# Optimization experiments

Measured on AMD Instinct MI355X. Metric: run time of the kernel, lower is better.

Reference implementation:

```python
import jax, jax.numpy as jnp
import numpy as np

HEAD_SIZE = 128  # matches init head_size; original scales by global head_size**-0.5


def setup_inputs() -> dict:
    key = jax.random.key(0)
    k1, k2, k3, k4 = jax.random.split(key, 4)
    B, T, C, D = 16, 2048, 1024, HEAD_SIZE
    x = jax.random.normal(k1, (B, T, C), dtype=jnp.float32)
    # torch Linear weight is [out,in]; store transposed so forward is x @ W
    Wq = jax.random.normal(k2, (C, D), dtype=jnp.float32) * (C ** -0.5)
    Wk = jax.random.normal(k3, (C, D), dtype=jnp.float32) * (C ** -0.5)
    Wv = jax.random.normal(k4, (C, D), dtype=jnp.float32) * (C ** -0.5)
    return {"x": x, "Wq": Wq, "Wk": Wk, "Wv": Wv}


def reference(x, Wq, Wk, Wv):
    # x: [B,T,C]; projections -> [B,T,D]
    q = x @ Wq
    k = x @ Wk
    v = x @ Wv
    T = x.shape[1]
    scale = HEAD_SIZE ** -0.5
    # scores: [B,T,T]
    wei = jnp.einsum("btd,bsd->bts", q, k) * scale
    causal = jnp.tril(jnp.ones((T, T), dtype=bool))  # tril buffer
    wei = jnp.where(causal, wei, -jnp.inf)
    wei = jax.nn.softmax(wei, axis=-1)
    # dropout is identity in eval mode (deterministic reference)
    return wei @ v  # [B,T,D]
```

## Files before the change

### kernel.cpp

```cpp
#include <hip/hip_runtime.h>
#include <hip/hip_bf16.h>

typedef short bf16x8 __attribute__((ext_vector_type(8)));
typedef float f32x4 __attribute__((ext_vector_type(4)));
typedef unsigned short u16x4 __attribute__((ext_vector_type(4)));

#define B_ 16
#define T_ 2048
#define C_ 1024
#define D_ 128
#define M_ (B_ * T_)

static __device__ __forceinline__ unsigned short f2bf(float f) {
    unsigned int u = __builtin_bit_cast(unsigned int, f);
    unsigned int r = (u + 0x7fffu + ((u >> 16) & 1u)) >> 16;
    return (unsigned short)r;
}

static __device__ __forceinline__ void gll16(const unsigned short* g, unsigned short* l) {
    __builtin_amdgcn_global_load_lds(
        (const __attribute__((address_space(1))) void*)g,
        (__attribute__((address_space(3))) void*)l, 16, 0, 0);
}

#define TPAD 133

__global__ void wt_kernel(const float* __restrict__ Wq, const float* __restrict__ Wk,
                          const float* __restrict__ Wv, unsigned short* __restrict__ Wt) {
    __shared__ float Tl[64 * TPAD];
    const int o  = blockIdx.x >> 4;
    const int k0 = (blockIdx.x & 15) * 64;
    const float* W = (o == 0) ? Wq : (o == 1) ? Wk : Wv;
    const int tid = threadIdx.x;

    const int kr = tid >> 5;
    const int n4 = (tid & 31) * 4;
#pragma unroll
    for (int j = 0; j < 8; ++j) {
        float4 v = *(const float4*)(W + (size_t)(k0 + kr + j * 8) * 128 + n4);
        *(float4*)&Tl[(kr + j * 8) * TPAD + n4] = v;
    }
    __syncthreads();

    const int nb = tid >> 3;
    const int kg = (tid & 7) * 8;
#pragma unroll
    for (int j = 0; j < 4; ++j) {
        const int nn = nb + j * 32;
        const int kk = kg ^ ((nn & 7) * 8);
        bf16x8 v;
#pragma unroll
        for (int e = 0; e < 8; ++e)
            v[e] = (short)f2bf(Tl[(kk + e) * TPAD + nn]);
        *(bf16x8*)&Wt[((size_t)o * 128 + nn) * 1024 + k0 + kg] = v;
    }
}

#define ASTR 68

__launch_bounds__(512, 2)
__global__ void qkv_kernel(const float* __restrict__ x, const unsigned short* __restrict__ Wt,
                           unsigned short* __restrict__ Q, unsigned short* __restrict__ K,
                           unsigned short* __restrict__ Vt) {
    __shared__ unsigned short Alds[2][128 * ASTR];
    __shared__ unsigned short Blds[2][384 * 64];

    const int tid  = threadIdx.x;
    const int lane = tid & 63;
    const int w    = tid >> 6;
    const int wr   = w >> 2;
    const int wc   = w & 3;
    const int lr   = lane & 15;
    const int lk   = lane >> 4;
    const int m0   = blockIdx.x * 128;

    const int axr = tid >> 4;
    const int axc = (tid & 15) * 4;

    float4 ar[4];
    auto loadA = [&](int k0) {
#pragma unroll
        for (int j = 0; j < 4; ++j)
            ar[j] = *(const float4*)(x + (size_t)(m0 + axr + j * 32) * C_ + k0 + axc);
    };
    auto writeA = [&](int buf) {
#pragma unroll
        for (int j = 0; j < 4; ++j) {
            u16x4 v;
            v[0] = f2bf(ar[j].x); v[1] = f2bf(ar[j].y);
            v[2] = f2bf(ar[j].z); v[3] = f2bf(ar[j].w);
            *(u16x4*)&Alds[buf][(axr + j * 32) * ASTR + axc] = v;
        }
    };

    auto stageB = [&](int k0, int buf) {
#pragma unroll
        for (int c = 0; c < 6; ++c) {
            const int chunk = w * 6 + c;
            const unsigned short* g = Wt + (size_t)(chunk * 8 + (lane >> 3)) * 1024
                                         + k0 + (lane & 7) * 8;
            gll16(g, &Blds[buf][chunk * 512]);
        }
    };

    f32x4 acc[4][6] = {};

    auto compute = [&](int buf) {
#pragma unroll
        for (int kk = 0; kk < 2; ++kk) {
            bf16x8 a[4], b[6];
#pragma unroll
            for (int rb = 0; rb < 4; ++rb)
                a[rb] = *(bf16x8*)&Alds[buf][(wr * 64 + rb * 16 + lr) * ASTR + kk * 32 + lk * 8];
#pragma unroll
            for (int nb = 0; nb < 6; ++nb) {
                const int ng = wc * 96 + nb * 16 + lr;
                b[nb] = *(bf16x8*)&Blds[buf][ng * 64 + ((kk * 32 + lk * 8) ^ ((ng & 7) * 8))];
            }
#pragma unroll
            for (int rb = 0; rb < 4; ++rb)
#pragma unroll
                for (int nb = 0; nb < 6; ++nb)
                    acc[rb][nb] = __builtin_amdgcn_mfma_f32_16x16x32_bf16(a[rb], b[nb], acc[rb][nb], 0, 0, 0);
        }
    };

    stageB(0, 0);
    loadA(0);
    writeA(0);

    for (int t = 0; t < 16; ++t) {
        __syncthreads();
        const int cur = t & 1;
        if (t < 15) {
            stageB((t + 1) * 64, cur ^ 1);
            loadA((t + 1) * 64);
        }
        compute(cur);
        if (t < 15) writeA(cur ^ 1);
    }

    const float qscale = 0.08838834764831845f;
    const int b  = m0 / T_;
    const int t0 = m0 % T_;
#pragma unroll
    for (int rb = 0; rb < 4; ++rb) {
#pragma unroll
        for (int nb = 0; nb < 6; ++nb) {
            const int row0 = wr * 64 + rb * 16 + lk * 4;
            const int col  = wc * 96 + nb * 16 + lr;
            const int o    = col >> 7;
            const int d    = col & 127;
            f32x4 a = acc[rb][nb];
            if (o == 0) {
#pragma unroll
                for (int r = 0; r < 4; ++r)
                    Q[(size_t)(m0 + row0 + r) * D_ + d] = f2bf(a[r] * qscale);
            } else if (o == 1) {
#pragma unroll
                for (int r = 0; r < 4; ++r)
                    K[(size_t)(m0 + row0 + r) * D_ + d] = f2bf(a[r]);
            } else {
                u16x4 pv;
#pragma unroll
                for (int r = 0; r < 4; ++r) pv[r] = f2bf(a[r]);
                *(u16x4*)&Vt[((size_t)b * D_ + d) * T_ + t0 + row0] = pv;
            }
        }
    }
}

#define KSTR 132
#define VSTR 68
#define PSTR 68

__launch_bounds__(256, 2)
__global__ void attn_kernel(const unsigned short* __restrict__ Q, const unsigned short* __restrict__ K,
                            const unsigned short* __restrict__ Vt, float* __restrict__ out) {
    __shared__ unsigned short Klds[2][64 * KSTR];
    __shared__ unsigned short Vlds[2][128 * VSTR];
    __shared__ unsigned short Plds[4][16 * PSTR];

    const int tid  = threadIdx.x;
    const int lane = tid & 63;
    const int w    = tid >> 6;
    const int lr   = lane & 15;
    const int lk   = lane >> 4;

    int bid = blockIdx.x;
    int batch, qt;
    if (bid < 256) { batch = bid >> 4; qt = bid & 15; }
    else           { bid -= 256; batch = bid >> 4; qt = 31 - (bid & 15); }

    const unsigned short* Qb = Q  + (size_t)batch * T_ * D_;
    const unsigned short* Kb = K  + (size_t)batch * T_ * D_;
    const unsigned short* Vb = Vt + (size_t)batch * D_ * T_;
    float* outb = out + (size_t)batch * T_ * D_;

    const int kxr = tid >> 4;
    const int kxc = (tid & 15) * 8;
    const int vxr = tid >> 3;
    const int vxc = (tid & 7) * 8;

    bf16x8 kr[4], vr[4];
    auto kv_load = [&](int kvt) {
        const int kv0 = kvt * 64;
#pragma unroll
        for (int j = 0; j < 4; ++j)
            kr[j] = *(const bf16x8*)(Kb + (size_t)(kv0 + kxr + j * 16) * D_ + kxc);
#pragma unroll
        for (int j = 0; j < 4; ++j)
            vr[j] = *(const bf16x8*)(Vb + (size_t)(vxr + j * 32) * T_ + kv0 + vxc);
    };
    auto kv_write = [&](int buf) {
#pragma unroll
        for (int j = 0; j < 4; ++j)
            *(bf16x8*)&Klds[buf][(kxr + j * 16) * KSTR + kxc] = kr[j];
#pragma unroll
        for (int j = 0; j < 4; ++j)
            *(bf16x8*)&Vlds[buf][(vxr + j * 32) * VSTR + vxc] = vr[j];
    };

    const int qw = qt * 64 + w * 16;

    bf16x8 qf[4];
#pragma unroll
    for (int c = 0; c < 4; ++c)
        qf[c] = *(const bf16x8*)(Qb + (size_t)(qw + lr) * D_ + lk * 8 + c * 32);

    f32x4 o_acc[8] = {};
    float mrun[4] = {-1e30f, -1e30f, -1e30f, -1e30f};
    float lrun[4] = {0.f, 0.f, 0.f, 0.f};

    kv_load(0);
    kv_write(0);

    for (int kvt = 0; kvt <= qt; ++kvt) {
        const int cur = kvt & 1;
        __syncthreads();
        if (kvt < qt) kv_load(kvt + 1);

        f32x4 s[4];
#pragma unroll
        for (int nb = 0; nb < 4; ++nb) {
            f32x4 a = {};
#pragma unroll
            for (int c = 0; c < 4; ++c) {
                bf16x8 kf = *(bf16x8*)&Klds[cur][(nb * 16 + lr) * KSTR + lk * 8 + c * 32];
                a = __builtin_amdgcn_mfma_f32_16x16x32_bf16(qf[c], kf, a, 0, 0, 0);
            }
            s[nb] = a;
        }

        if (kvt == qt) {
#pragma unroll
            for (int nb = 0; nb < 4; ++nb)
#pragma unroll
                for (int r = 0; r < 4; ++r) {
                    int qg = qw + lk * 4 + r;
                    int kg = kvt * 64 + nb * 16 + lr;
                    if (kg > qg) s[nb][r] = -1e30f;
                }
        }

        float scale_[4];
#pragma unroll
        for (int r = 0; r < 4; ++r) {
            float mx = fmaxf(fmaxf(s[0][r], s[1][r]), fmaxf(s[2][r], s[3][r]));
            mx = fmaxf(mx, __shfl_xor(mx, 1));
            mx = fmaxf(mx, __shfl_xor(mx, 2));
            mx = fmaxf(mx, __shfl_xor(mx, 4));
            mx = fmaxf(mx, __shfl_xor(mx, 8));
            float mnew = fmaxf(mrun[r], mx);
            scale_[r]  = __expf(mrun[r] - mnew);
            mrun[r]    = mnew;
            lrun[r]   *= scale_[r];
        }
#pragma unroll
        for (int db = 0; db < 8; ++db)
#pragma unroll
            for (int r = 0; r < 4; ++r) o_acc[db][r] *= scale_[r];

#pragma unroll
        for (int nb = 0; nb < 4; ++nb)
#pragma unroll
            for (int r = 0; r < 4; ++r) {
                float p = __expf(s[nb][r] - mrun[r]);
                lrun[r] += p;
                Plds[w][(lk * 4 + r) * PSTR + nb * 16 + lr] = f2bf(p);
            }
        asm volatile("s_waitcnt lgkmcnt(0)" ::: "memory");
        __builtin_amdgcn_sched_barrier(0);

        bf16x8 pa[2];
#pragma unroll
        for (int c = 0; c < 2; ++c)
            pa[c] = *(bf16x8*)&Plds[w][lr * PSTR + lk * 8 + c * 32];
#pragma unroll
        for (int db = 0; db < 8; ++db) {
            f32x4 oo = o_acc[db];
#pragma unroll
            for (int c = 0; c < 2; ++c) {
                bf16x8 vf = *(bf16x8*)&Vlds[cur][(db * 16 + lr) * VSTR + lk * 8 + c * 32];
                oo = __builtin_amdgcn_mfma_f32_16x16x32_bf16(pa[c], vf, oo, 0, 0, 0);
            }
            o_acc[db] = oo;
        }

        if (kvt < qt) kv_write(cur ^ 1);
    }

#pragma unroll
    for (int r = 0; r < 4; ++r) {
        float sgm = lrun[r];
        sgm += __shfl_xor(sgm, 1);
        sgm += __shfl_xor(sgm, 2);
        sgm += __shfl_xor(sgm, 4);
        sgm += __shfl_xor(sgm, 8);
        lrun[r] = 1.0f / sgm;
    }
#pragma unroll
    for (int db = 0; db < 8; ++db)
#pragma unroll
        for (int r = 0; r < 4; ++r)
            outb[(size_t)(qw + lk * 4 + r) * D_ + db * 16 + lr] = o_acc[db][r] * lrun[r];
}

extern "C" void kernel_launch(void* const* d_in, const int* in_sizes, int n_in,
                              void* d_out, int out_size, void* d_ws, size_t ws_size,
                              hipStream_t stream) {
    const float* x  = (const float*)d_in[0];
    const float* Wq = (const float*)d_in[1];
    const float* Wk = (const float*)d_in[2];
    const float* Wv = (const float*)d_in[3];

    unsigned short* Wt  = (unsigned short*)d_ws;
    unsigned short* Qw  = (unsigned short*)((char*)d_ws + (1 << 20));
    unsigned short* Kw  = Qw + (size_t)M_ * D_;
    unsigned short* Vtw = Kw + (size_t)M_ * D_;

    hipLaunchKernelGGL(wt_kernel, dim3(48), dim3(256), 0, stream, Wq, Wk, Wv, Wt);
    hipLaunchKernelGGL(qkv_kernel, dim3(256), dim3(512), 0, stream, x, Wt, Qw, Kw, Vtw);
    hipLaunchKernelGGL(attn_kernel, dim3(512), dim3(256), 0, stream, Qw, Kw, Vtw, (float*)d_out);
}
```

Measured before the change: 105.8 us.

## Restructure QKV projection: full-K x tile in LDS, weights pre-tiled for direct MFMA loads

The weight-prep kernel now writes the bf16 weights in a fragment-tiled layout so each lane can load its MFMA B operand straight from global memory (L2-resident) without staging in LDS. The QKV kernel now loads a 64-row slab of x over the full K dimension, converts it to bf16 in LDS once, and runs the whole K loop with no double buffering or per-step barriers. The grid doubles to 512 blocks of 64 rows, and each wave computes 48 output columns. This removes the per-iteration sync and staging overhead. In exchange it uses about 131KB of LDS per block (one block per CU), does not overlap the x load with compute, and makes every block re-read all weights from cache.

```diff
diff --git a/kernel.cpp b/kernel.cpp
--- a/kernel.cpp
+++ b/kernel.cpp
@@ -17,16 +17,10 @@
     return (unsigned short)r;
 }
 
-static __device__ __forceinline__ void gll16(const unsigned short* g, unsigned short* l) {
-    __builtin_amdgcn_global_load_lds(
-        (const __attribute__((address_space(1))) void*)g,
-        (__attribute__((address_space(3))) void*)l, 16, 0, 0);
-}
-
 #define TPAD 133
 
 __global__ void wt_kernel(const float* __restrict__ Wq, const float* __restrict__ Wk,
-                          const float* __restrict__ Wv, unsigned short* __restrict__ Wt) {
+                          const float* __restrict__ Wv, unsigned short* __restrict__ Wt2) {
     __shared__ float Tl[64 * TPAD];
     const int o  = blockIdx.x >> 4;
     const int k0 = (blockIdx.x & 15) * 64;
@@ -42,102 +36,62 @@
     }
     __syncthreads();
 
-    const int nb = tid >> 3;
-    const int kg = (tid & 7) * 8;
+    const int n    = tid & 127;
+    const int half = tid >> 7;
 #pragma unroll
     for (int j = 0; j < 4; ++j) {
-        const int nn = nb + j * 32;
-        const int kk = kg ^ ((nn & 7) * 8);
+        const int kg = half * 4 + j;
         bf16x8 v;
 #pragma unroll
         for (int e = 0; e < 8; ++e)
-            v[e] = (short)f2bf(Tl[(kk + e) * TPAD + nn]);
-        *(bf16x8*)&Wt[((size_t)o * 128 + nn) * 1024 + k0 + kg] = v;
-    }
-}
-
-#define ASTR 68
-
-__launch_bounds__(512, 2)
-__global__ void qkv_kernel(const float* __restrict__ x, const unsigned short* __restrict__ Wt,
+            v[e] = (short)f2bf(Tl[(kg * 8 + e) * TPAD + n]);
+        const int nblk = o * 8 + (n >> 4);
+        const int kblk = (k0 >> 3) + kg;
+        *(bf16x8*)&Wt2[((size_t)nblk * 128 + kblk) * 128 + (n & 15) * 8] = v;
+    }
+}
+
+#define XSTR 1026
+
+__launch_bounds__(512, 1)
+__global__ void qkv_kernel(const float* __restrict__ x, const unsigned short* __restrict__ Wt2,
                            unsigned short* __restrict__ Q, unsigned short* __restrict__ K,
                            unsigned short* __restrict__ Vt) {
-    __shared__ unsigned short Alds[2][128 * ASTR];
-    __shared__ unsigned short Blds[2][384 * 64];
+    __shared__ unsigned short X[64 * XSTR];
 
     const int tid  = threadIdx.x;
     const int lane = tid & 63;
     const int w    = tid >> 6;
-    const int wr   = w >> 2;
-    const int wc   = w & 3;
     const int lr   = lane & 15;
     const int lk   = lane >> 4;
-    const int m0   = blockIdx.x * 128;
-
-    const int axr = tid >> 4;
-    const int axc = (tid & 15) * 4;
-
-    float4 ar[4];
-    auto loadA = [&](int k0) {
-#pragma unroll
-        for (int j = 0; j < 4; ++j)
-            ar[j] = *(const float4*)(x + (size_t)(m0 + axr + j * 32) * C_ + k0 + axc);
-    };
-    auto writeA = [&](int buf) {
-#pragma unroll
-        for (int j = 0; j < 4; ++j) {
-            u16x4 v;
-            v[0] = f2bf(ar[j].x); v[1] = f2bf(ar[j].y);
-            v[2] = f2bf(ar[j].z); v[3] = f2bf(ar[j].w);
-            *(u16x4*)&Alds[buf][(axr + j * 32) * ASTR + axc] = v;
-        }
-    };
-
-    auto stageB = [&](int k0, int buf) {
-#pragma unroll
-        for (int c = 0; c < 6; ++c) {
-            const int chunk = w * 6 + c;
-            const unsigned short* g = Wt + (size_t)(chunk * 8 + (lane >> 3)) * 1024
-                                         + k0 + (lane & 7) * 8;
-            gll16(g, &Blds[buf][chunk * 512]);
-        }
-    };
-
-    f32x4 acc[4][6] = {};
-
-    auto compute = [&](int buf) {
-#pragma unroll
-        for (int kk = 0; kk < 2; ++kk) {
-            bf16x8 a[4], b[6];
-#pragma unroll
-            for (int rb = 0; rb < 4; ++rb)
-                a[rb] = *(bf16x8*)&Alds[buf][(wr * 64 + rb * 16 + lr) * ASTR + kk * 32 + lk * 8];
-#pragma unroll
-            for (int nb = 0; nb < 6; ++nb) {
-                const int ng = wc * 96 + nb * 16 + lr;
-                b[nb] = *(bf16x8*)&Blds[buf][ng * 64 + ((kk * 32 + lk * 8) ^ ((ng & 7) * 8))];
-            }
-#pragma unroll
-            for (int rb = 0; rb < 4; ++rb)
-#pragma unroll
-                for (int nb = 0; nb < 6; ++nb)
-                    acc[rb][nb] = __builtin_amdgcn_mfma_f32_16x16x32_bf16(a[rb], b[nb], acc[rb][nb], 0, 0, 0);
-        }
-    };
-
-    stageB(0, 0);
-    loadA(0);
-    writeA(0);
-
-    for (int t = 0; t < 16; ++t) {
-        __syncthreads();
-        const int cur = t & 1;
-        if (t < 15) {
-            stageB((t + 1) * 64, cur ^ 1);
-            loadA((t + 1) * 64);
-        }
-        compute(cur);
-        if (t < 15) writeA(cur ^ 1);
+    const int m0   = blockIdx.x * 64;
+
+#pragma unroll 8
+    for (int j = 0; j < 32; ++j) {
+        const int idx = tid + j * 512;
+        const int row = idx >> 8;
+        const int c4  = idx & 255;
+        float4 v = *(const float4*)(x + (size_t)(m0 + row) * C_ + c4 * 4);
+        u16x4 h;
+        h[0] = f2bf(v.x); h[1] = f2bf(v.y); h[2] = f2bf(v.z); h[3] = f2bf(v.w);
+        *(u16x4*)&X[row * XSTR + c4 * 4] = h;
+    }
+    __syncthreads();
+
+    f32x4 acc[4][3] = {};
+    for (int ko = 0; ko < 32; ++ko) {
+        bf16x8 a[4], b[3];
+#pragma unroll
+        for (int nb = 0; nb < 3; ++nb)
+            b[nb] = *(const bf16x8*)(Wt2 + ((size_t)(w * 3 + nb) * 128 + ko * 4 + lk) * 128 + lr * 8);
+#pragma unroll
+        for (int rb = 0; rb < 4; ++rb)
+            a[rb] = *(bf16x8*)&X[(rb * 16 + lr) * XSTR + ko * 32 + lk * 8];
+#pragma unroll
+        for (int rb = 0; rb < 4; ++rb)
+#pragma unroll
+            for (int nb = 0; nb < 3; ++nb)
+                acc[rb][nb] = __builtin_amdgcn_mfma_f32_16x16x32_bf16(a[rb], b[nb], acc[rb][nb], 0, 0, 0);
     }
 
     const float qscale = 0.08838834764831845f;
@@ -146,9 +100,9 @@
 #pragma unroll
     for (int rb = 0; rb < 4; ++rb) {
 #pragma unroll
-        for (int nb = 0; nb < 6; ++nb) {
-            const int row0 = wr * 64 + rb * 16 + lk * 4;
-            const int col  = wc * 96 + nb * 16 + lr;
+        for (int nb = 0; nb < 3; ++nb) {
+            const int row0 = rb * 16 + lk * 4;
+            const int col  = w * 48 + nb * 16 + lr;
             const int o    = col >> 7;
             const int d    = col & 127;
             f32x4 a = acc[rb][nb];
@@ -334,12 +288,12 @@
     const float* Wk = (const float*)d_in[2];
     const float* Wv = (const float*)d_in[3];
 
-    unsigned short* Wt  = (unsigned short*)d_ws;
+    unsigned short* Wt2 = (unsigned short*)d_ws;
     unsigned short* Qw  = (unsigned short*)((char*)d_ws + (1 << 20));
     unsigned short* Kw  = Qw + (size_t)M_ * D_;
     unsigned short* Vtw = Kw + (size_t)M_ * D_;
 
-    hipLaunchKernelGGL(wt_kernel, dim3(48), dim3(256), 0, stream, Wq, Wk, Wv, Wt);
-    hipLaunchKernelGGL(qkv_kernel, dim3(256), dim3(512), 0, stream, x, Wt, Qw, Kw, Vtw);
+    hipLaunchKernelGGL(wt_kernel, dim3(48), dim3(256), 0, stream, Wq, Wk, Wv, Wt2);
+    hipLaunchKernelGGL(qkv_kernel, dim3(512), dim3(512), 0, stream, x, Wt2, Qw, Kw, Vtw);
     hipLaunchKernelGGL(attn_kernel, dim3(512), dim3(256), 0, stream, Qw, Kw, Vtw, (float*)d_out);
 }
```

Result: slower. 126.9 us (+20.0%).

## Pre-convert x to swizzled bf16 and split QKV GEMM into 128x128 tiles

Applied to the files above, without the earlier changes.

Adds a separate kernel that converts x from fp32 to bf16 in a swizzled layout. The QKV projection then stages both operands straight into LDS with global_load_lds, and the grid becomes 768 blocks of 256 threads, each computing one 128x128 output tile (one of Q, K or V). This removes the in-kernel fp32-to-bf16 conversion and register staging, and raises occupancy. In exchange it adds an extra full write and read of a 64MB bf16 copy of x, makes each bf16 row of x get read by three blocks, and drops the double-buffered prefetch in favour of a synchronous load-then-compute loop.

```diff
diff --git a/kernel.cpp b/kernel.cpp
--- a/kernel.cpp
+++ b/kernel.cpp
@@ -21,6 +21,25 @@
     __builtin_amdgcn_global_load_lds(
         (const __attribute__((address_space(1))) void*)g,
         (__attribute__((address_space(3))) void*)l, 16, 0, 0);
+}
+
+__global__ void cvt_kernel(const float* __restrict__ x, unsigned short* __restrict__ xb) {
+    int idx = blockIdx.x * 256 + threadIdx.x;
+#pragma unroll
+    for (int it = 0; it < 4; ++it, idx += 1048576) {
+        const int row = idx >> 7;
+        const int g   = idx & 127;
+        const int gs  = (g & ~7) | ((g & 7) ^ (row & 7));
+        const float* src = x + (size_t)row * C_ + g * 8;
+        float4 v0 = *(const float4*)src;
+        float4 v1 = *(const float4*)(src + 4);
+        bf16x8 h;
+        h[0] = (short)f2bf(v0.x); h[1] = (short)f2bf(v0.y);
+        h[2] = (short)f2bf(v0.z); h[3] = (short)f2bf(v0.w);
+        h[4] = (short)f2bf(v1.x); h[5] = (short)f2bf(v1.y);
+        h[6] = (short)f2bf(v1.z); h[7] = (short)f2bf(v1.w);
+        *(bf16x8*)&xb[(size_t)row * C_ + gs * 8] = h;
+    }
 }
 
 #define TPAD 133
@@ -56,88 +75,62 @@
     }
 }
 
-#define ASTR 68
-
-__launch_bounds__(512, 2)
-__global__ void qkv_kernel(const float* __restrict__ x, const unsigned short* __restrict__ Wt,
+__launch_bounds__(256, 3)
+__global__ void qkv_kernel(const unsigned short* __restrict__ xb, const unsigned short* __restrict__ Wt,
                            unsigned short* __restrict__ Q, unsigned short* __restrict__ K,
                            unsigned short* __restrict__ Vt) {
-    __shared__ unsigned short Alds[2][128 * ASTR];
-    __shared__ unsigned short Blds[2][384 * 64];
+    __shared__ unsigned short Alds[128 * 64];
+    __shared__ unsigned short Blds[128 * 64];
 
     const int tid  = threadIdx.x;
     const int lane = tid & 63;
     const int w    = tid >> 6;
-    const int wr   = w >> 2;
-    const int wc   = w & 3;
+    const int wr   = w >> 1;
+    const int wc   = w & 1;
     const int lr   = lane & 15;
     const int lk   = lane >> 4;
-    const int m0   = blockIdx.x * 128;
-
-    const int axr = tid >> 4;
-    const int axc = (tid & 15) * 4;
-
-    float4 ar[4];
-    auto loadA = [&](int k0) {
-#pragma unroll
-        for (int j = 0; j < 4; ++j)
-            ar[j] = *(const float4*)(x + (size_t)(m0 + axr + j * 32) * C_ + k0 + axc);
-    };
-    auto writeA = [&](int buf) {
+
+    const int nt = blockIdx.x >> 8;
+    const int mt = blockIdx.x & 255;
+    const int m0 = mt * 128;
+    const int n0 = nt * 128;
+
+    const int srow = tid >> 3;
+    const int sg   = (tid & 7) * 8;
+
+    f32x4 acc[4][4] = {};
+
+    for (int t = 0; t < 16; ++t) {
+        const int k0 = t * 64;
 #pragma unroll
         for (int j = 0; j < 4; ++j) {
-            u16x4 v;
-            v[0] = f2bf(ar[j].x); v[1] = f2bf(ar[j].y);
-            v[2] = f2bf(ar[j].z); v[3] = f2bf(ar[j].w);
-            *(u16x4*)&Alds[buf][(axr + j * 32) * ASTR + axc] = v;
-        }
-    };
-
-    auto stageB = [&](int k0, int buf) {
-#pragma unroll
-        for (int c = 0; c < 6; ++c) {
-            const int chunk = w * 6 + c;
-            const unsigned short* g = Wt + (size_t)(chunk * 8 + (lane >> 3)) * 1024
-                                         + k0 + (lane & 7) * 8;
-            gll16(g, &Blds[buf][chunk * 512]);
-        }
-    };
-
-    f32x4 acc[4][6] = {};
-
-    auto compute = [&](int buf) {
+            gll16(xb + (size_t)(m0 + j * 32 + srow) * C_ + k0 + sg,
+                  &Alds[(j * 32 + w * 8) * 64]);
+            gll16(Wt + (size_t)(n0 + j * 32 + srow) * C_ + k0 + sg,
+                  &Blds[(j * 32 + w * 8) * 64]);
+        }
+        __syncthreads();
+
 #pragma unroll
         for (int kk = 0; kk < 2; ++kk) {
-            bf16x8 a[4], b[6];
+            bf16x8 a[4], b[4];
+#pragma unroll
+            for (int rb = 0; rb < 4; ++rb) {
+                const int row = wr * 64 + rb * 16 + lr;
+                a[rb] = *(bf16x8*)&Alds[row * 64 + ((kk * 32 + lk * 8) ^ ((row & 7) * 8))];
+            }
+#pragma unroll
+            for (int nb = 0; nb < 4; ++nb) {
+                const int row = wc * 64 + nb * 16 + lr;
+                b[nb] = *(bf16x8*)&Blds[row * 64 + ((kk * 32 + lk * 8) ^ ((row & 7) * 8))];
+            }
 #pragma unroll
             for (int rb = 0; rb < 4; ++rb)
-                a[rb] = *(bf16x8*)&Alds[buf][(wr * 64 + rb * 16 + lr) * ASTR + kk * 32 + lk * 8];
-#pragma unroll
-            for (int nb = 0; nb < 6; ++nb) {
-                const int ng = wc * 96 + nb * 16 + lr;
-                b[nb] = *(bf16x8*)&Blds[buf][ng * 64 + ((kk * 32 + lk * 8) ^ ((ng & 7) * 8))];
-            }
-#pragma unroll
-            for (int rb = 0; rb < 4; ++rb)
-#pragma unroll
-                for (int nb = 0; nb < 6; ++nb)
+#pragma unroll
+                for (int nb = 0; nb < 4; ++nb)
                     acc[rb][nb] = __builtin_amdgcn_mfma_f32_16x16x32_bf16(a[rb], b[nb], acc[rb][nb], 0, 0, 0);
         }
-    };
-
-    stageB(0, 0);
-    loadA(0);
-    writeA(0);
-
-    for (int t = 0; t < 16; ++t) {
         __syncthreads();
-        const int cur = t & 1;
-        if (t < 15) {
-            stageB((t + 1) * 64, cur ^ 1);
-            loadA((t + 1) * 64);
-        }
-        compute(cur);
-        if (t < 15) writeA(cur ^ 1);
     }
 
     const float qscale = 0.08838834764831845f;
@@ -146,17 +139,15 @@
 #pragma unroll
     for (int rb = 0; rb < 4; ++rb) {
 #pragma unroll
-        for (int nb = 0; nb < 6; ++nb) {
+        for (int nb = 0; nb < 4; ++nb) {
             const int row0 = wr * 64 + rb * 16 + lk * 4;
-            const int col  = wc * 96 + nb * 16 + lr;
-            const int o    = col >> 7;
-            const int d    = col & 127;
+            const int d    = wc * 64 + nb * 16 + lr;
             f32x4 a = acc[rb][nb];
-            if (o == 0) {
+            if (nt == 0) {
 #pragma unroll
                 for (int r = 0; r < 4; ++r)
                     Q[(size_t)(m0 + row0 + r) * D_ + d] = f2bf(a[r] * qscale);
-            } else if (o == 1) {
+            } else if (nt == 1) {
 #pragma unroll
                 for (int r = 0; r < 4; ++r)
                     K[(size_t)(m0 + row0 + r) * D_ + d] = f2bf(a[r]);
@@ -334,12 +325,14 @@
     const float* Wk = (const float*)d_in[2];
     const float* Wv = (const float*)d_in[3];
 
-    unsigned short* Wt  = (unsigned short*)d_ws;
-    unsigned short* Qw  = (unsigned short*)((char*)d_ws + (1 << 20));
+    unsigned short* xb  = (unsigned short*)d_ws;
+    unsigned short* Wt  = (unsigned short*)((char*)d_ws + (64u << 20));
+    unsigned short* Qw  = (unsigned short*)((char*)d_ws + (65u << 20));
     unsigned short* Kw  = Qw + (size_t)M_ * D_;
     unsigned short* Vtw = Kw + (size_t)M_ * D_;
 
+    hipLaunchKernelGGL(cvt_kernel, dim3(4096), dim3(256), 0, stream, x, xb);
     hipLaunchKernelGGL(wt_kernel, dim3(48), dim3(256), 0, stream, Wq, Wk, Wv, Wt);
-    hipLaunchKernelGGL(qkv_kernel, dim3(256), dim3(512), 0, stream, x, Wt, Qw, Kw, Vtw);
+    hipLaunchKernelGGL(qkv_kernel, dim3(768), dim3(256), 0, stream, xb, Wt, Qw, Kw, Vtw);
     hipLaunchKernelGGL(attn_kernel, dim3(512), dim3(256), 0, stream, Qw, Kw, Vtw, (float*)d_out);
 }
```

Result: slower. 118.7 us (+12.2%).
